# Optimization experiments

Hardware: AMD Instinct MI355X
Metric: run time of the kernel (lower is better)

## Reference

```python
import jax, jax.numpy as jnp
import numpy as np

K_SIZE = 3
STRIDE = 1
PAD = 1


def setup_inputs() -> dict:
    key = jax.random.key(0)
    k1, k2 = jax.random.split(key)
    x = jax.random.normal(k1, (32, 32, 128, 128), dtype=jnp.float32)
    # torch param shape: (kernel_size, kernel_size, in_channels, out_channels)
    kernel = jax.random.normal(k2, (3, 3, 32, 64), dtype=jnp.float32)
    return {"x": x, "kernel": kernel}


def reference(x, kernel):
    # Faithful to the original: patches are flattened in (c, ki, kj) order while
    # the kernel is flattened via .view(-1, out) in (ki, kj, c) order. The
    # effective weight seen by the matmul is therefore the raw (K,K,C,O) buffer
    # REINTERPRETED as (C,K,K,O) (a reshape, not a transpose).
    O = kernel.shape[-1]
    C = kernel.shape[2]
    w_eff = kernel.reshape(C, K_SIZE, K_SIZE, O)       # (C, kh, kw, O), same buffer order
    w_oihw = jnp.transpose(w_eff, (3, 0, 1, 2))        # (O, C, kh, kw)
    out = jax.lax.conv_general_dilated(
        x, w_oihw,
        window_strides=(STRIDE, STRIDE),
        padding=[(PAD, PAD), (PAD, PAD)],
        dimension_numbers=("NCHW", "OIHW", "NCHW"),
    )
    return out
```

## Files before the change

### kernel.cpp

```cpp
#include <hip/hip_runtime.h>

typedef __attribute__((ext_vector_type(8))) short   bf16x8;
typedef __attribute__((ext_vector_type(4))) float   f32x4;
typedef __attribute__((ext_vector_type(4))) unsigned int u32x4;

#define HT    8
#define WT    32
#define WSPAN 34
#define NR    10

__device__ __forceinline__ unsigned short f2bf(float f) {
    union { float f; unsigned u; } v; v.f = f;
    unsigned u = v.u;
    u += 0x7FFFu + ((u >> 16) & 1u);
    return (unsigned short)(u >> 16);
}

__global__ __launch_bounds__(256, 4)
void conv3x3_fused(const float* __restrict__ x, const float* __restrict__ wk,
                   float* __restrict__ out) {
    const int hb = blockIdx.x, wq4 = blockIdx.y, n = blockIdx.z;
    const int H0 = hb * HT, W0 = wq4 * WT;
    const int tid  = threadIdx.x;
    const int lane = tid & 63, wid = tid >> 6;
    const int lq = lane >> 4, lr = lane & 15;

    __shared__ u32x4 lds[NR * WSPAN * 4];

    const bool act = (tid < 136);
    const int cb = (tid < 128) ? (tid >> 5) : ((tid - 128) >> 1);
    const int wq = (tid < 128) ? (tid & 31) : (32 + ((tid - 128) & 1));

    auto issue_loads = [&](int rg, float (&dst)[8]) {
        const int wg = W0 - 1 + wq;
        const bool ok = act && ((unsigned)rg < 128u) && ((unsigned)wg < 128u);
        const float* p = x + (((n * 32 + cb * 8) * 128 + rg) * 128 + wg);
        #pragma unroll
        for (int j = 0; j < 8; ++j)
            dst[j] = ok ? p[j * 16384] : 0.0f;
    };
    auto lds_write = [&](int row, const float (&src)[8]) {
        if (!act) return;
        const int f = (wq >> 1) & 3;
        u32x4 pk;
        pk[0] = (unsigned)f2bf(src[0]) | ((unsigned)f2bf(src[1]) << 16);
        pk[1] = (unsigned)f2bf(src[2]) | ((unsigned)f2bf(src[3]) << 16);
        pk[2] = (unsigned)f2bf(src[4]) | ((unsigned)f2bf(src[5]) << 16);
        pk[3] = (unsigned)f2bf(src[6]) | ((unsigned)f2bf(src[7]) << 16);
        lds[(row * WSPAN + wq) * 4 + (cb ^ f)] = pk;
    };
    auto frag_read = [&](int row, int w) -> bf16x8 {
        const int f = (w >> 1) & 3;
        union { u32x4 u; bf16x8 v; } cv;
        cv.u = lds[(row * WSPAN + w) * 4 + (lq ^ f)];
        return cv.v;
    };

    float buf[2][8];
    issue_loads(H0 - 1, buf[0]);
    issue_loads(H0,     buf[1]);

#define STAGE(R)                                                              \
    {                                                                         \
        lds_write((R), buf[(R) & 1]);                                         \
        if ((R) + 2 < NR) issue_loads(H0 + (R) + 1, buf[(R) & 1]);            \
    }
    STAGE(0) STAGE(1) STAGE(2) STAGE(3) STAGE(4)
    STAGE(5) STAGE(6) STAGE(7) STAGE(8) STAGE(9)
#undef STAGE

    bf16x8 wA[9];
    #pragma unroll
    for (int p = 0; p < 9; ++p) {
        const int ki = p / 3, kj = p % 3;
        union { bf16x8 v; unsigned short s[8]; } u;
        #pragma unroll
        for (int j = 0; j < 8; ++j) {
            const int c = lq * 8 + j;
            u.s[j] = f2bf(wk[((c * 3 + ki) * 3 + kj) * 64 + wid * 16 + lr]);
        }
        wA[p] = u.v;
    }

    __syncthreads();

    f32x4 acc[3][2];
    const f32x4 zero = {0.f, 0.f, 0.f, 0.f};
    #pragma unroll
    for (int a = 0; a < 3; ++a)
        #pragma unroll
        for (int pg = 0; pg < 2; ++pg) acc[a][pg] = zero;

    float* obase = out + (((size_t)(n * 64 + wid * 16 + lq * 4) * 128) * 128) + W0 + lr;

#define ROW(RHO)                                                              \
    {                                                                         \
        _Pragma("unroll")                                                     \
        for (int pg = 0; pg < 2; ++pg) {                                      \
            const bf16x8 fb0 = frag_read((RHO), pg * 16 + lr + 0);            \
            const bf16x8 fb1 = frag_read((RHO), pg * 16 + lr + 1);            \
            const bf16x8 fb2 = frag_read((RHO), pg * 16 + lr + 2);            \
            _Pragma("unroll")                                                 \
            for (int ki = 0; ki < 3; ++ki) {                                  \
                if ((RHO) - ki < 0 || (RHO) - ki > HT - 1) continue;          \
                const int a = ((RHO) - ki + 1) % 3;                           \
                acc[a][pg] = __builtin_amdgcn_mfma_f32_16x16x32_bf16(         \
                    wA[ki * 3 + 0], fb0, acc[a][pg], 0, 0, 0);                \
                acc[a][pg] = __builtin_amdgcn_mfma_f32_16x16x32_bf16(         \
                    wA[ki * 3 + 1], fb1, acc[a][pg], 0, 0, 0);                \
                acc[a][pg] = __builtin_amdgcn_mfma_f32_16x16x32_bf16(         \
                    wA[ki * 3 + 2], fb2, acc[a][pg], 0, 0, 0);                \
            }                                                                 \
        }                                                                     \
        if ((RHO) >= 2) {                                                     \
            const int h = H0 + (RHO) - 2;                                     \
            const int a = ((RHO) - 1) % 3;                                    \
            _Pragma("unroll")                                                 \
            for (int pg = 0; pg < 2; ++pg) {                                  \
                _Pragma("unroll")                                             \
                for (int j = 0; j < 4; ++j)                                   \
                    obase[(j * 128 + h) * 128 + pg * 16] = acc[a][pg][j];     \
                acc[a][pg] = zero;                                            \
            }                                                                 \
        }                                                                     \
    }

    ROW(0) ROW(1) ROW(2) ROW(3) ROW(4) ROW(5) ROW(6) ROW(7) ROW(8) ROW(9)
#undef ROW
}

extern "C" void kernel_launch(void* const* d_in, const int* in_sizes, int n_in,
                              void* d_out, int out_size, void* d_ws, size_t ws_size,
                              hipStream_t stream) {
    const float* x  = (const float*)d_in[0];
    const float* wk = (const float*)d_in[1];
    float* out = (float*)d_out;
    dim3 grid(16, 4, 32);
    dim3 block(256);
    conv3x3_fused<<<grid, block, 0, stream>>>(x, wk, out);
}
```

Baseline: 43.17 us.

## Spread halo tile loading across all 256 threads with deeper prefetch

The staging of the input tile is rebalanced so that all 256 threads take part. Each half-block now loads alternate rows, and halo columns are spread over 40 threads per half. Previously 136 threads did all the loading in a 2-deep pipeline. The change issues more global loads up front to raise memory-level parallelism, at the cost of more live registers (five 8-float buffers).

```diff
diff --git a/kernel.cpp b/kernel.cpp
--- a/kernel.cpp
+++ b/kernel.cpp
@@ -27,27 +27,27 @@
 
     __shared__ u32x4 lds[NR * WSPAN * 4];
 
-    const bool act = (tid < 136);
-    const int cb = (tid < 128) ? (tid >> 5) : ((tid - 128) >> 1);
-    const int wq = (tid < 128) ? (tid & 31) : (32 + ((tid - 128) & 1));
+    const int pairId = tid >> 7, t = tid & 127;
+    const int cb = t >> 5, wq = t & 31;
+    const bool hasH = (t < 40);
+    const int hk = t >> 3, hcb = (t & 7) >> 1, hwq = 32 + (t & 1);
 
-    auto issue_loads = [&](int rg, float (&dst)[8]) {
-        const int wg = W0 - 1 + wq;
-        const bool ok = act && ((unsigned)rg < 128u) && ((unsigned)wg < 128u);
-        const float* p = x + (((n * 32 + cb * 8) * 128 + rg) * 128 + wg);
+    auto issue_loads = [&](int rg, int icb, int iwq, float (&dst)[8]) {
+        const int wg = W0 - 1 + iwq;
+        const bool ok = ((unsigned)rg < 128u) && ((unsigned)wg < 128u);
+        const float* p = x + (((n * 32 + icb * 8) * 128 + rg) * 128 + wg);
         #pragma unroll
         for (int j = 0; j < 8; ++j)
             dst[j] = ok ? p[j * 16384] : 0.0f;
     };
-    auto lds_write = [&](int row, const float (&src)[8]) {
-        if (!act) return;
-        const int f = (wq >> 1) & 3;
+    auto lds_write = [&](int row, int icb, int iwq, const float (&src)[8]) {
+        const int f = (iwq >> 1) & 3;
         u32x4 pk;
         pk[0] = (unsigned)f2bf(src[0]) | ((unsigned)f2bf(src[1]) << 16);
         pk[1] = (unsigned)f2bf(src[2]) | ((unsigned)f2bf(src[3]) << 16);
         pk[2] = (unsigned)f2bf(src[4]) | ((unsigned)f2bf(src[5]) << 16);
         pk[3] = (unsigned)f2bf(src[6]) | ((unsigned)f2bf(src[7]) << 16);
-        lds[(row * WSPAN + wq) * 4 + (cb ^ f)] = pk;
+        lds[(row * WSPAN + iwq) * 4 + (icb ^ f)] = pk;
     };
     auto frag_read = [&](int row, int w) -> bf16x8 {
         const int f = (w >> 1) & 3;
@@ -56,18 +56,20 @@
         return cv.v;
     };
 
-    float buf[2][8];
-    issue_loads(H0 - 1, buf[0]);
-    issue_loads(H0,     buf[1]);
+    float buf[4][8], hbuf[8];
+    issue_loads(H0 - 1 + pairId,     cb, wq, buf[0]);
+    issue_loads(H0 - 1 + pairId + 2, cb, wq, buf[1]);
+    issue_loads(H0 - 1 + pairId + 4, cb, wq, buf[2]);
+    issue_loads(H0 - 1 + pairId + 6, cb, wq, buf[3]);
+    if (hasH) issue_loads(H0 - 1 + 2 * hk + pairId, hcb, hwq, hbuf);
 
-#define STAGE(R)                                                              \
-    {                                                                         \
-        lds_write((R), buf[(R) & 1]);                                         \
-        if ((R) + 2 < NR) issue_loads(H0 + (R) + 1, buf[(R) & 1]);            \
-    }
-    STAGE(0) STAGE(1) STAGE(2) STAGE(3) STAGE(4)
-    STAGE(5) STAGE(6) STAGE(7) STAGE(8) STAGE(9)
-#undef STAGE
+    lds_write(0 + pairId, cb, wq, buf[0]);
+    issue_loads(H0 - 1 + pairId + 8, cb, wq, buf[0]);
+    lds_write(2 + pairId, cb, wq, buf[1]);
+    lds_write(4 + pairId, cb, wq, buf[2]);
+    lds_write(6 + pairId, cb, wq, buf[3]);
+    lds_write(8 + pairId, cb, wq, buf[0]);
+    if (hasH) lds_write(2 * hk + pairId, hcb, hwq, hbuf);
 
     bf16x8 wA[9];
     #pragma unroll
```

Result: slower. 44.08 us (+2.1%).

## Process two row tiles per block with double-buffered LDS staging

Applied to the files above, without the earlier changes.

Each block now handles 16 output rows instead of 8, split into two halves with separate LDS buffers. While the MFMA work for the first half runs, the global loads and bf16 conversion for the second half are issued and written into the second buffer, overlapping memory traffic with compute. This also amortizes the weight load and conversion over twice as many rows, and halves the grid. The cost is double the LDS footprint, an occupancy hint lowered from 4 to 3 blocks, and fewer blocks to spread across CUs.

```diff
diff --git a/kernel.cpp b/kernel.cpp
--- a/kernel.cpp
+++ b/kernel.cpp
@@ -8,6 +8,7 @@
 #define WT    32
 #define WSPAN 34
 #define NR    10
+#define HALF  (NR * WSPAN * 4)
 
 __device__ __forceinline__ unsigned short f2bf(float f) {
     union { float f; unsigned u; } v; v.f = f;
@@ -16,16 +17,16 @@
     return (unsigned short)(u >> 16);
 }
 
-__global__ __launch_bounds__(256, 4)
+__global__ __launch_bounds__(256, 3)
 void conv3x3_fused(const float* __restrict__ x, const float* __restrict__ wk,
                    float* __restrict__ out) {
-    const int hb = blockIdx.x, wq4 = blockIdx.y, n = blockIdx.z;
-    const int H0 = hb * HT, W0 = wq4 * WT;
+    const int hb2 = blockIdx.x, wq4 = blockIdx.y, n = blockIdx.z;
+    const int H0 = hb2 * 16, W0 = wq4 * WT;
     const int tid  = threadIdx.x;
     const int lane = tid & 63, wid = tid >> 6;
     const int lq = lane >> 4, lr = lane & 15;
 
-    __shared__ u32x4 lds[NR * WSPAN * 4];
+    __shared__ u32x4 lds[2 * HALF];
 
     const bool act = (tid < 136);
     const int cb = (tid < 128) ? (tid >> 5) : ((tid - 128) >> 1);
@@ -39,7 +40,7 @@
         for (int j = 0; j < 8; ++j)
             dst[j] = ok ? p[j * 16384] : 0.0f;
     };
-    auto lds_write = [&](int row, const float (&src)[8]) {
+    auto lds_write = [&](int half, int row, const float (&src)[8]) {
         if (!act) return;
         const int f = (wq >> 1) & 3;
         u32x4 pk;
@@ -47,12 +48,12 @@
         pk[1] = (unsigned)f2bf(src[2]) | ((unsigned)f2bf(src[3]) << 16);
         pk[2] = (unsigned)f2bf(src[4]) | ((unsigned)f2bf(src[5]) << 16);
         pk[3] = (unsigned)f2bf(src[6]) | ((unsigned)f2bf(src[7]) << 16);
-        lds[(row * WSPAN + wq) * 4 + (cb ^ f)] = pk;
+        lds[half * HALF + (row * WSPAN + wq) * 4 + (cb ^ f)] = pk;
     };
-    auto frag_read = [&](int row, int w) -> bf16x8 {
+    auto frag_read = [&](int half, int row, int w) -> bf16x8 {
         const int f = (w >> 1) & 3;
         union { u32x4 u; bf16x8 v; } cv;
-        cv.u = lds[(row * WSPAN + w) * 4 + (lq ^ f)];
+        cv.u = lds[half * HALF + (row * WSPAN + w) * 4 + (lq ^ f)];
         return cv.v;
     };
 
@@ -60,14 +61,14 @@
     issue_loads(H0 - 1, buf[0]);
     issue_loads(H0,     buf[1]);
 
-#define STAGE(R)                                                              \
+#define STAGE(HF, BASE, R)                                                    \
     {                                                                         \
-        lds_write((R), buf[(R) & 1]);                                         \
-        if ((R) + 2 < NR) issue_loads(H0 + (R) + 1, buf[(R) & 1]);            \
+        lds_write((HF), (R), buf[(R) & 1]);                                   \
+        if ((R) + 2 < NR) issue_loads((BASE) + (R) + 1, buf[(R) & 1]);        \
     }
-    STAGE(0) STAGE(1) STAGE(2) STAGE(3) STAGE(4)
-    STAGE(5) STAGE(6) STAGE(7) STAGE(8) STAGE(9)
-#undef STAGE
+    STAGE(0, H0, 0) STAGE(0, H0, 1) STAGE(0, H0, 2) STAGE(0, H0, 3)
+    STAGE(0, H0, 4) STAGE(0, H0, 5) STAGE(0, H0, 6) STAGE(0, H0, 7)
+    STAGE(0, H0, 8) STAGE(0, H0, 9)
 
     bf16x8 wA[9];
     #pragma unroll
@@ -82,8 +83,6 @@
         wA[p] = u.v;
     }
 
-    __syncthreads();
-
     f32x4 acc[3][2];
     const f32x4 zero = {0.f, 0.f, 0.f, 0.f};
     #pragma unroll
@@ -93,13 +92,13 @@
 
     float* obase = out + (((size_t)(n * 64 + wid * 16 + lq * 4) * 128) * 128) + W0 + lr;
 
-#define ROW(RHO)                                                              \
+#define ROW(HF, TOFF, RHO)                                                    \
     {                                                                         \
         _Pragma("unroll")                                                     \
         for (int pg = 0; pg < 2; ++pg) {                                      \
-            const bf16x8 fb0 = frag_read((RHO), pg * 16 + lr + 0);            \
-            const bf16x8 fb1 = frag_read((RHO), pg * 16 + lr + 1);            \
-            const bf16x8 fb2 = frag_read((RHO), pg * 16 + lr + 2);            \
+            const bf16x8 fb0 = frag_read((HF), (RHO), pg * 16 + lr + 0);      \
+            const bf16x8 fb1 = frag_read((HF), (RHO), pg * 16 + lr + 1);      \
+            const bf16x8 fb2 = frag_read((HF), (RHO), pg * 16 + lr + 2);      \
             _Pragma("unroll")                                                 \
             for (int ki = 0; ki < 3; ++ki) {                                  \
                 if ((RHO) - ki < 0 || (RHO) - ki > HT - 1) continue;          \
@@ -113,7 +112,7 @@
             }                                                                 \
         }                                                                     \
         if ((RHO) >= 2) {                                                     \
-            const int h = H0 + (RHO) - 2;                                     \
+            const int h = H0 + (TOFF) + (RHO) - 2;                            \
             const int a = ((RHO) - 1) % 3;                                    \
             _Pragma("unroll")                                                 \
             for (int pg = 0; pg < 2; ++pg) {                                  \
@@ -125,8 +124,27 @@
         }                                                                     \
     }
 
-    ROW(0) ROW(1) ROW(2) ROW(3) ROW(4) ROW(5) ROW(6) ROW(7) ROW(8) ROW(9)
+    __syncthreads();
+
+    issue_loads(H0 + 7, buf[0]);
+    issue_loads(H0 + 8, buf[1]);
+    STAGE(1, H0 + 8, 0) ROW(0, 0, 0)
+    STAGE(1, H0 + 8, 1) ROW(0, 0, 1)
+    STAGE(1, H0 + 8, 2) ROW(0, 0, 2)
+    STAGE(1, H0 + 8, 3) ROW(0, 0, 3)
+    STAGE(1, H0 + 8, 4) ROW(0, 0, 4)
+    STAGE(1, H0 + 8, 5) ROW(0, 0, 5)
+    STAGE(1, H0 + 8, 6) ROW(0, 0, 6)
+    STAGE(1, H0 + 8, 7) ROW(0, 0, 7)
+    STAGE(1, H0 + 8, 8) ROW(0, 0, 8)
+    STAGE(1, H0 + 8, 9) ROW(0, 0, 9)
+
+    __syncthreads();
+
+    ROW(1, 8, 0) ROW(1, 8, 1) ROW(1, 8, 2) ROW(1, 8, 3) ROW(1, 8, 4)
+    ROW(1, 8, 5) ROW(1, 8, 6) ROW(1, 8, 7) ROW(1, 8, 8) ROW(1, 8, 9)
 #undef ROW
+#undef STAGE
 }
 
 extern "C" void kernel_launch(void* const* d_in, const int* in_sizes, int n_in,
@@ -135,7 +153,7 @@
     const float* x  = (const float*)d_in[0];
     const float* wk = (const float*)d_in[1];
     float* out = (float*)d_out;
-    dim3 grid(16, 4, 32);
+    dim3 grid(8, 4, 32);
     dim3 block(256);
     conv3x3_fused<<<grid, block, 0, stream>>>(x, wk, out);
 }
```

New measurement: 72.42 us. +67.7%, slower.
